# Kernel optimization log

Measured on AMD Instinct MI355X. Metric: run time of the kernel, lower is better.

The kernel has to match this reference:

```python
import jax, jax.numpy as jnp
import numpy as np

B, T, I, H, C = 32, 1024, 512, 1024, 512

def setup_inputs() -> dict:
    key = jax.random.key(0)
    ks = jax.random.split(key, 9)
    s_ih = 1.0 / np.sqrt(H)
    inp = {
        "x": jax.random.normal(ks[0], (B, T, I), dtype=jnp.float32),
        # LSTMCell params (PyTorch layout: [4H, in], gate order i,f,g,o)
        "W_ih": jax.random.uniform(ks[1], (4 * H, I), minval=-s_ih, maxval=s_ih, dtype=jnp.float32),
        "W_hh": jax.random.uniform(ks[2], (4 * H, H), minval=-s_ih, maxval=s_ih, dtype=jnp.float32),
        "b_ih": jax.random.uniform(ks[3], (4 * H,), minval=-s_ih, maxval=s_ih, dtype=jnp.float32),
        "b_hh": jax.random.uniform(ks[4], (4 * H,), minval=-s_ih, maxval=s_ih, dtype=jnp.float32),
        # fc head [C, H]
        "fc_w": jax.random.uniform(ks[5], (C, H), minval=-s_ih, maxval=s_ih, dtype=jnp.float32),
        "fc_b": jax.random.uniform(ks[6], (C,), minval=-s_ih, maxval=s_ih, dtype=jnp.float32),
        # ln_hidden [H, H] (reverse=False branch)
        "ln_w": jax.random.uniform(ks[7], (H, H), minval=-s_ih, maxval=s_ih, dtype=jnp.float32),
        "ln_b": jax.random.uniform(ks[8], (H,), minval=-s_ih, maxval=s_ih, dtype=jnp.float32),
    }
    return inp

def _lstm_forward(x, W_ih, W_hh, b_ih, b_hh):
    # Pre-compute input contribution for all timesteps: [B,T,4H]
    x_gates = jnp.einsum('bti,gi->btg', x, W_ih) + b_ih
    h0 = jnp.zeros((x.shape[0], H), dtype=x.dtype)
    c0 = jnp.zeros((x.shape[0], H), dtype=x.dtype)

    def step(carry, xg_t):
        h, c = carry
        gates = xg_t + h @ W_hh.T + b_hh  # [B,4H]
        i, f, g, o = jnp.split(gates, 4, axis=-1)
        c = jax.nn.sigmoid(f) * c + jax.nn.sigmoid(i) * jnp.tanh(g)
        h = jax.nn.sigmoid(o) * jnp.tanh(c)
        return (h, c), h

    (_, _), hs = jax.lax.scan(step, (h0, c0), jnp.swapaxes(x_gates, 0, 1))  # hs: [T,B,H]
    return jnp.swapaxes(hs, 0, 1)  # [B,T,H]

def reference(x, W_ih, W_hh, b_ih, b_hh, fc_w, fc_b, ln_w, ln_b):
    outputs = _lstm_forward(x, W_ih, W_hh, b_ih, b_hh)  # [B,T,H]
    out = jnp.einsum('bth,ch->btc', outputs, fc_w) + fc_b  # [B,T,C]
    # Faithful quirk: torch.stack(outputs, 1) on a [B,T,H] tensor -> [T,B,H]
    states_t = jnp.swapaxes(outputs, 0, 1)  # [T,B,H]
    states = jnp.einsum('tbh,gh->tbg', states_t, ln_w) + ln_b  # [T,B,H]
    return (out, states)
```

## Files before the change

kernel.cpp:

```cpp
#include <hip/hip_runtime.h>
#include <stdint.h>

#define B_  32
#define T_  1024
#define I_  512
#define H_  1024
#define C_  512
#define G4H 4096
#define NWG 128

typedef __bf16 bf16x8 __attribute__((ext_vector_type(8)));
typedef float  f32x4  __attribute__((ext_vector_type(4)));
typedef unsigned long long u64;

__device__ __forceinline__ unsigned short f2bf(float f) {
    uint32_t b = __float_as_uint(f);
    b = (b + 0x7FFFu + ((b >> 16) & 1u)) >> 16;
    return (unsigned short)b;
}
__device__ __forceinline__ float sigf(float x)   { return 1.0f / (1.0f + __expf(-x)); }
__device__ __forceinline__ float tanh_f(float x) { return 2.0f / (1.0f + __expf(-2.0f * x)) - 1.0f; }

__global__ void cvt_kernel(const float* __restrict__ src, unsigned short* __restrict__ dst, int n4) {
    int i = blockIdx.x * blockDim.x + threadIdx.x;
    if (i < n4) {
        float4 v = ((const float4*)src)[i];
        ushort4 o;
        o.x = f2bf(v.x); o.y = f2bf(v.y); o.z = f2bf(v.z); o.w = f2bf(v.w);
        ((ushort4*)dst)[i] = o;
    }
}

__global__ void cvt_x_kernel(const float* __restrict__ src, unsigned short* __restrict__ dst) {
    int i4 = blockIdx.x * blockDim.x + threadIdx.x;
    int b   = i4 / (T_ * I_ / 4);
    int rem = i4 % (T_ * I_ / 4);
    int t   = rem / (I_ / 4);
    int c4  = rem % (I_ / 4);
    float4 v = ((const float4*)src)[i4];
    ushort4 o;
    o.x = f2bf(v.x); o.y = f2bf(v.y); o.z = f2bf(v.z); o.w = f2bf(v.w);
    ((ushort4*)dst)[(t * B_ + b) * (I_ / 4) + c4] = o;
}

__global__ void bias_kernel(const float* __restrict__ a, const float* __restrict__ b, float* __restrict__ o) {
    int i = blockIdx.x * blockDim.x + threadIdx.x;
    if (i < G4H) o[i] = a[i] + b[i];
}

__global__ __launch_bounds__(512, 1) void lstm_rec(
        const unsigned short* __restrict__ whh,
        const unsigned short* __restrict__ wih,
        const unsigned short* __restrict__ xb,
        const float* __restrict__ bias,
        unsigned short* __restrict__ hall,
        unsigned int* __restrict__ flags)
{
    extern __shared__ char smem[];
    unsigned short* Wlds    = (unsigned short*)smem;
    float*          scratch = (float*)(smem + 98304);
    unsigned short* hstage  = (unsigned short*)(smem + 98304 + 32768);

    const int tid  = threadIdx.x;
    const int wg   = blockIdx.x;
    const int lane = tid & 63;
    const int wq   = tid >> 6;
    const int l15  = lane & 15;
    const int l4   = lane >> 4;

    for (int s = tid; s < 32 * 192; s += 512) {
        int col = s / 192, g = s % 192;
        int grow = (col >> 3) * H_ + wg * 8 + (col & 7);
        const unsigned short* src = (g < 128) ? (whh + grow * H_ + g * 8)
                                              : (wih + grow * I_ + (g - 128) * 8);
        int4 v = *(const int4*)src;
        int gd = g ^ (col & 7);
        *(int4*)(Wlds + col * 1536 + gd * 8) = v;
    }
    float bs0 = 0.f, bs1 = 0.f, bs2 = 0.f, bs3 = 0.f;
    if (tid < 256) {
        int u = tid & 7;
        bs0 = bias[0 * H_ + wg * 8 + u];
        bs1 = bias[1 * H_ + wg * 8 + u];
        bs2 = bias[2 * H_ + wg * 8 + u];
        bs3 = bias[3 * H_ + wg * 8 + u];
    }
    __syncthreads();

    float c_state = 0.0f;

    for (int t = 0; t < T_; ++t) {
        f32x4 acc[2][2];
        #pragma unroll
        for (int a = 0; a < 2; a++)
            #pragma unroll
            for (int b = 0; b < 2; b++) acc[a][b] = (f32x4){0.f, 0.f, 0.f, 0.f};

        #pragma unroll
        for (int kxs = 0; kxs < 2; kxs++) {
            int kk = wq * 64 + kxs * 32 + l4 * 8;
            bf16x8 af[2];
            #pragma unroll
            for (int mt = 0; mt < 2; mt++) {
                int bb = mt * 16 + l15;
                af[mt] = *(const bf16x8*)(xb + ((size_t)t * B_ + bb) * I_ + kk);
            }
            int gbase = 128 + (kk >> 3);
            bf16x8 bfr[2];
            #pragma unroll
            for (int nt = 0; nt < 2; nt++) {
                int col = nt * 16 + l15;
                int gg = gbase ^ (col & 7);
                bfr[nt] = *(const bf16x8*)(Wlds + col * 1536 + gg * 8);
            }
            #pragma unroll
            for (int mt = 0; mt < 2; mt++)
                #pragma unroll
                for (int nt = 0; nt < 2; nt++)
                    acc[mt][nt] = __builtin_amdgcn_mfma_f32_16x16x32_bf16(af[mt], bfr[nt], acc[mt][nt], 0, 0, 0);
        }

        if (t > 0) {
            if (tid < NWG) {
                const unsigned int* f = flags + ((size_t)(t - 1) * NWG + tid) * 16;
                while (__hip_atomic_load(f, __ATOMIC_RELAXED, __HIP_MEMORY_SCOPE_AGENT) == 0u)
                    __builtin_amdgcn_s_sleep(1);
            }
            __syncthreads();
            asm volatile("" ::: "memory");
        }

        const unsigned short* hprev = hall + (size_t)t * (B_ * H_);
        #pragma unroll
        for (int khs = 0; khs < 4; khs++) {
            int kk = wq * 128 + khs * 32 + l4 * 8;
            bf16x8 af[2];
            #pragma unroll
            for (int mt = 0; mt < 2; mt++) {
                int bb = mt * 16 + l15;
                af[mt] = *(const bf16x8*)(hprev + bb * H_ + kk);
            }
            int gbase = kk >> 3;
            bf16x8 bfr[2];
            #pragma unroll
            for (int nt = 0; nt < 2; nt++) {
                int col = nt * 16 + l15;
                int gg = gbase ^ (col & 7);
                bfr[nt] = *(const bf16x8*)(Wlds + col * 1536 + gg * 8);
            }
            #pragma unroll
            for (int mt = 0; mt < 2; mt++)
                #pragma unroll
                for (int nt = 0; nt < 2; nt++)
                    acc[mt][nt] = __builtin_amdgcn_mfma_f32_16x16x32_bf16(af[mt], bfr[nt], acc[mt][nt], 0, 0, 0);
        }

        float* myscr = scratch + wq * 1024;
        #pragma unroll
        for (int mt = 0; mt < 2; mt++)
            #pragma unroll
            for (int nt = 0; nt < 2; nt++)
                #pragma unroll
                for (int r = 0; r < 4; r++) {
                    int bb  = mt * 16 + l4 * 4 + r;
                    int col = nt * 16 + l15;
                    myscr[bb * 32 + (col ^ ((bb & 7) << 2))] = acc[mt][nt][r];
                }
        __syncthreads();

        if (tid < 256) {
            int bb = tid >> 3, u = tid & 7;
            int sw = (bb & 7) << 2;
            float p0 = bs0, p1 = bs1, p2 = bs2, p3 = bs3;
            const float* base = scratch + bb * 32;
            #pragma unroll
            for (int q = 0; q < 8; q++) {
                const float* sc = base + q * 1024;
                p0 += sc[(u)      ^ sw];
                p1 += sc[(8 + u)  ^ sw];
                p2 += sc[(16 + u) ^ sw];
                p3 += sc[(24 + u) ^ sw];
            }
            float ig = sigf(p0), fg = sigf(p1), gg = tanh_f(p2), og = sigf(p3);
            c_state = fg * c_state + ig * gg;
            float h = og * tanh_f(c_state);
            hstage[bb * 8 + u] = f2bf(h);
        }
        __syncthreads();

        if (tid < 64) {
            int bb = tid >> 1, part = tid & 1;
            u64 q = *(u64*)(hstage + bb * 8 + part * 4);
            u64* dst = (u64*)(hall + ((size_t)(t + 1) * B_ + bb) * H_ + wg * 8 + part * 4);
            __hip_atomic_store(dst, q, __ATOMIC_RELAXED, __HIP_MEMORY_SCOPE_AGENT);
        }
        __syncthreads();
        if (tid == 0)
            __hip_atomic_store(flags + ((size_t)t * NWG + wg) * 16, 1u,
                               __ATOMIC_RELAXED, __HIP_MEMORY_SCOPE_AGENT);
    }
}

template<int PERM>
__global__ __launch_bounds__(256) void gemm_bt(
        const unsigned short* __restrict__ A,
        const unsigned short* __restrict__ Bw,
        const float* __restrict__ bias,
        float* __restrict__ out)
{
    __shared__ unsigned short As[128 * 64];
    __shared__ unsigned short Bs[128 * 64];
    const int tid  = threadIdx.x;
    const int lane = tid & 63, w = tid >> 6;
    const int wm = w >> 1, wn = w & 1;
    const int mbase = blockIdx.y * 128, nbase = blockIdx.x * 128;
    const int l15 = lane & 15, l4 = lane >> 4;

    f32x4 acc[4][4];
    #pragma unroll
    for (int i = 0; i < 4; i++)
        #pragma unroll
        for (int j = 0; j < 4; j++) acc[i][j] = (f32x4){0.f, 0.f, 0.f, 0.f};

    for (int kb = 0; kb < 16; kb++) {
        __syncthreads();
        #pragma unroll
        for (int i = 0; i < 4; i++) {
            int s = i * 256 + tid;
            int row = s >> 3, g = s & 7;
            int gd = g ^ (row & 7);
            int4 va = *(const int4*)(A  + (size_t)(mbase + row) * 1024 + kb * 64 + g * 8);
            *(int4*)(As + row * 64 + gd * 8) = va;
            int4 vb = *(const int4*)(Bw + (size_t)(nbase + row) * 1024 + kb * 64 + g * 8);
            *(int4*)(Bs + row * 64 + gd * 8) = vb;
        }
        __syncthreads();
        #pragma unroll
        for (int kk = 0; kk < 2; kk++) {
            bf16x8 af[4], bf[4];
            #pragma unroll
            for (int mt = 0; mt < 4; mt++) {
                int row = wm * 64 + mt * 16 + l15;
                int gg = (kk * 4 + l4) ^ (row & 7);
                af[mt] = *(const bf16x8*)(As + row * 64 + gg * 8);
            }
            #pragma unroll
            for (int nt = 0; nt < 4; nt++) {
                int row = wn * 64 + nt * 16 + l15;
                int gg = (kk * 4 + l4) ^ (row & 7);
                bf[nt] = *(const bf16x8*)(Bs + row * 64 + gg * 8);
            }
            #pragma unroll
            for (int mt = 0; mt < 4; mt++)
                #pragma unroll
                for (int nt = 0; nt < 4; nt++)
                    acc[mt][nt] = __builtin_amdgcn_mfma_f32_16x16x32_bf16(af[mt], bf[nt], acc[mt][nt], 0, 0, 0);
        }
    }
    #pragma unroll
    for (int mt = 0; mt < 4; mt++)
        #pragma unroll
        for (int nt = 0; nt < 4; nt++)
            #pragma unroll
            for (int r = 0; r < 4; r++) {
                int grow = mbase + wm * 64 + mt * 16 + l4 * 4 + r;
                int gcol = nbase + wn * 64 + nt * 16 + l15;
                float v = acc[mt][nt][r] + bias[gcol];
                int idx;
                if (PERM == 1) {
                    int tt = grow >> 5, bb = grow & 31;
                    idx = (bb * 1024 + tt) * 512 + gcol;
                } else {
                    idx = grow * 1024 + gcol;
                }
                out[idx] = v;
            }
}

extern "C" void kernel_launch(void* const* d_in, const int* in_sizes, int n_in,
                              void* d_out, int out_size, void* d_ws, size_t ws_size,
                              hipStream_t stream) {
    (void)in_sizes; (void)n_in; (void)out_size; (void)ws_size;
    const float* x    = (const float*)d_in[0];
    const float* Wih  = (const float*)d_in[1];
    const float* Whh  = (const float*)d_in[2];
    const float* bih  = (const float*)d_in[3];
    const float* bhh  = (const float*)d_in[4];
    const float* fcw  = (const float*)d_in[5];
    const float* fcb  = (const float*)d_in[6];
    const float* lnw  = (const float*)d_in[7];
    const float* lnb  = (const float*)d_in[8];
    float* out = (float*)d_out;

    char* ws = (char*)d_ws;
    size_t o = 0;
    unsigned short* whh_b = (unsigned short*)(ws + o); o += 8388608;
    unsigned short* wih_b = (unsigned short*)(ws + o); o += 4194304;
    unsigned short* fcw_b = (unsigned short*)(ws + o); o += 1048576;
    unsigned short* lnw_b = (unsigned short*)(ws + o); o += 2097152;
    unsigned short* x_b   = (unsigned short*)(ws + o); o += 33554432;
    float*          bias_c = (float*)(ws + o);         o += 16384;
    unsigned short* hall  = (unsigned short*)(ws + o); o += 67174400;
    unsigned int*   flags = (unsigned int*)(ws + o);   o += 8388608;

    hipMemsetAsync(flags, 0, 8388608, stream);
    hipMemsetAsync(hall, 0, 65536, stream);

    cvt_kernel<<<4096,  256, 0, stream>>>(Whh, whh_b, 4194304 / 4);
    cvt_kernel<<<2048,  256, 0, stream>>>(Wih, wih_b, 2097152 / 4);
    cvt_kernel<<<512,   256, 0, stream>>>(fcw, fcw_b, 524288 / 4);
    cvt_kernel<<<1024,  256, 0, stream>>>(lnw, lnw_b, 1048576 / 4);
    cvt_x_kernel<<<16384, 256, 0, stream>>>(x, x_b);
    bias_kernel<<<16, 256, 0, stream>>>(bih, bhh, bias_c);

    const unsigned short* a0 = whh_b;
    const unsigned short* a1 = wih_b;
    const unsigned short* a2 = x_b;
    const float*          a3 = bias_c;
    unsigned short*       a4 = hall;
    unsigned int*         a5 = flags;
    void* args[6] = { (void*)&a0, (void*)&a1, (void*)&a2, (void*)&a3, (void*)&a4, (void*)&a5 };
    hipLaunchCooperativeKernel((void*)lstm_rec, dim3(NWG), dim3(512), args,
                               (unsigned)(98304 + 32768 + 512), stream);

    const unsigned short* hseq = hall + 32768;
    gemm_bt<1><<<dim3(4, 256), 256, 0, stream>>>(hseq, fcw_b, fcb, out);
    gemm_bt<2><<<dim3(8, 256), 256, 0, stream>>>(hseq, lnw_b, lnb, out + 16777216);
}
```

Before: 4.450 ms.

## Cut per-step barriers in LSTM recurrence with per-wave polling and counter

The W_ih slice now lives in registers rather than LDS, which shrinks the weight tile and frees LDS for a double-buffered scratch area indexed by timestep parity. Each wave now polls its own 16 producer flags instead of the block polling and then hitting a barrier. The two trailing barriers are replaced by per-wave stores of h, followed by an LDS atomic counter whose last arriver publishes the block's flag. This shortens the serial critical path of every timestep, at the cost of relying on subtle memory ordering (relaxed atomics, manual waitcnt) that may be fragile.

```diff
diff --git a/kernel.cpp b/kernel.cpp
--- a/kernel.cpp
+++ b/kernel.cpp
@@ -58,8 +58,9 @@
 {
     extern __shared__ char smem[];
     unsigned short* Wlds    = (unsigned short*)smem;
-    float*          scratch = (float*)(smem + 98304);
-    unsigned short* hstage  = (unsigned short*)(smem + 98304 + 32768);
+    float*          scratch = (float*)(smem + 65536);
+    unsigned short* hstage  = (unsigned short*)(smem + 131072);
+    int*            done    = (int*)(smem + 131584);
 
     const int tid  = threadIdx.x;
     const int wg   = blockIdx.x;
@@ -68,15 +69,22 @@
     const int l15  = lane & 15;
     const int l4   = lane >> 4;
 
-    for (int s = tid; s < 32 * 192; s += 512) {
-        int col = s / 192, g = s % 192;
+    for (int s = tid; s < 32 * 128; s += 512) {
+        int col = s >> 7, g = s & 127;
         int grow = (col >> 3) * H_ + wg * 8 + (col & 7);
-        const unsigned short* src = (g < 128) ? (whh + grow * H_ + g * 8)
-                                              : (wih + grow * I_ + (g - 128) * 8);
-        int4 v = *(const int4*)src;
-        int gd = g ^ (col & 7);
-        *(int4*)(Wlds + col * 1536 + gd * 8) = v;
-    }
+        int4 v = *(const int4*)(whh + (size_t)grow * H_ + g * 8);
+        *(int4*)(Wlds + col * 1024 + (g ^ (col & 7)) * 8) = v;
+    }
+    bf16x8 wfx[2][2];
+    #pragma unroll
+    for (int kxs = 0; kxs < 2; kxs++)
+        #pragma unroll
+        for (int nt = 0; nt < 2; nt++) {
+            int col = nt * 16 + l15;
+            int grow = (col >> 3) * H_ + wg * 8 + (col & 7);
+            int kk = wq * 64 + kxs * 32 + l4 * 8;
+            wfx[kxs][nt] = *(const bf16x8*)(wih + (size_t)grow * I_ + kk);
+        }
     float bs0 = 0.f, bs1 = 0.f, bs2 = 0.f, bs3 = 0.f;
     if (tid < 256) {
         int u = tid & 7;
@@ -85,6 +93,7 @@
         bs2 = bias[2 * H_ + wg * 8 + u];
         bs3 = bias[3 * H_ + wg * 8 + u];
     }
+    if (tid == 0) *done = 0;
     __syncthreads();
 
     float c_state = 0.0f;
@@ -105,13 +114,39 @@
                 int bb = mt * 16 + l15;
                 af[mt] = *(const bf16x8*)(xb + ((size_t)t * B_ + bb) * I_ + kk);
             }
-            int gbase = 128 + (kk >> 3);
+            #pragma unroll
+            for (int mt = 0; mt < 2; mt++)
+                #pragma unroll
+                for (int nt = 0; nt < 2; nt++)
+                    acc[mt][nt] = __builtin_amdgcn_mfma_f32_16x16x32_bf16(af[mt], wfx[kxs][nt], acc[mt][nt], 0, 0, 0);
+        }
+
+        if (t > 0) {
+            if (lane < 16) {
+                const unsigned int* f = flags + ((size_t)(t - 1) * NWG + wq * 16 + lane) * 16;
+                while (__hip_atomic_load(f, __ATOMIC_RELAXED, __HIP_MEMORY_SCOPE_AGENT) == 0u)
+                    __builtin_amdgcn_s_sleep(1);
+            }
+            asm volatile("" ::: "memory");
+        }
+
+        const unsigned short* hprev = hall + (size_t)t * (B_ * H_);
+        #pragma unroll
+        for (int khs = 0; khs < 4; khs++) {
+            int kk = wq * 128 + khs * 32 + l4 * 8;
+            bf16x8 af[2];
+            #pragma unroll
+            for (int mt = 0; mt < 2; mt++) {
+                int bb = mt * 16 + l15;
+                af[mt] = *(const bf16x8*)(hprev + bb * H_ + kk);
+            }
+            int gbase = kk >> 3;
             bf16x8 bfr[2];
             #pragma unroll
             for (int nt = 0; nt < 2; nt++) {
                 int col = nt * 16 + l15;
                 int gg = gbase ^ (col & 7);
-                bfr[nt] = *(const bf16x8*)(Wlds + col * 1536 + gg * 8);
+                bfr[nt] = *(const bf16x8*)(Wlds + col * 1024 + gg * 8);
             }
             #pragma unroll
             for (int mt = 0; mt < 2; mt++)
@@ -120,42 +155,7 @@
                     acc[mt][nt] = __builtin_amdgcn_mfma_f32_16x16x32_bf16(af[mt], bfr[nt], acc[mt][nt], 0, 0, 0);
         }
 
-        if (t > 0) {
-            if (tid < NWG) {
-                const unsigned int* f = flags + ((size_t)(t - 1) * NWG + tid) * 16;
-                while (__hip_atomic_load(f, __ATOMIC_RELAXED, __HIP_MEMORY_SCOPE_AGENT) == 0u)
-                    __builtin_amdgcn_s_sleep(1);
-            }
-            __syncthreads();
-            asm volatile("" ::: "memory");
-        }
-
-        const unsigned short* hprev = hall + (size_t)t * (B_ * H_);
-        #pragma unroll
-        for (int khs = 0; khs < 4; khs++) {
-            int kk = wq * 128 + khs * 32 + l4 * 8;
-            bf16x8 af[2];
-            #pragma unroll
-            for (int mt = 0; mt < 2; mt++) {
-                int bb = mt * 16 + l15;
-                af[mt] = *(const bf16x8*)(hprev + bb * H_ + kk);
-            }
-            int gbase = kk >> 3;
-            bf16x8 bfr[2];
-            #pragma unroll
-            for (int nt = 0; nt < 2; nt++) {
-                int col = nt * 16 + l15;
-                int gg = gbase ^ (col & 7);
-                bfr[nt] = *(const bf16x8*)(Wlds + col * 1536 + gg * 8);
-            }
-            #pragma unroll
-            for (int mt = 0; mt < 2; mt++)
-                #pragma unroll
-                for (int nt = 0; nt < 2; nt++)
-                    acc[mt][nt] = __builtin_amdgcn_mfma_f32_16x16x32_bf16(af[mt], bfr[nt], acc[mt][nt], 0, 0, 0);
-        }
-
-        float* myscr = scratch + wq * 1024;
+        float* myscr = scratch + (t & 1) * 8192 + wq * 1024;
         #pragma unroll
         for (int mt = 0; mt < 2; mt++)
             #pragma unroll
@@ -172,7 +172,7 @@
             int bb = tid >> 3, u = tid & 7;
             int sw = (bb & 7) << 2;
             float p0 = bs0, p1 = bs1, p2 = bs2, p3 = bs3;
-            const float* base = scratch + bb * 32;
+            const float* base = scratch + (t & 1) * 8192 + bb * 32;
             #pragma unroll
             for (int q = 0; q < 8; q++) {
                 const float* sc = base + q * 1024;
@@ -185,19 +185,22 @@
             c_state = fg * c_state + ig * gg;
             float h = og * tanh_f(c_state);
             hstage[bb * 8 + u] = f2bf(h);
-        }
-        __syncthreads();
-
-        if (tid < 64) {
-            int bb = tid >> 1, part = tid & 1;
-            u64 q = *(u64*)(hstage + bb * 8 + part * 4);
-            u64* dst = (u64*)(hall + ((size_t)(t + 1) * B_ + bb) * H_ + wg * 8 + part * 4);
-            __hip_atomic_store(dst, q, __ATOMIC_RELAXED, __HIP_MEMORY_SCOPE_AGENT);
-        }
-        __syncthreads();
-        if (tid == 0)
-            __hip_atomic_store(flags + ((size_t)t * NWG + wg) * 16, 1u,
-                               __ATOMIC_RELAXED, __HIP_MEMORY_SCOPE_AGENT);
+            asm volatile("s_waitcnt lgkmcnt(0)" ::: "memory");
+
+            if (lane < 16) {
+                int pb = wq * 8 + (lane >> 1), part = lane & 1;
+                u64 q = *(const u64*)(hstage + pb * 8 + part * 4);
+                u64* dst = (u64*)(hall + ((size_t)(t + 1) * B_ + pb) * H_ + wg * 8 + part * 4);
+                __hip_atomic_store(dst, q, __ATOMIC_RELAXED, __HIP_MEMORY_SCOPE_AGENT);
+            }
+            asm volatile("s_waitcnt vmcnt(0)" ::: "memory");
+            if (lane == 0) {
+                int old = __hip_atomic_fetch_add(done, 1, __ATOMIC_RELAXED, __HIP_MEMORY_SCOPE_WORKGROUP);
+                if (old == t * 4 + 3)
+                    __hip_atomic_store(flags + ((size_t)t * NWG + wg) * 16, 1u,
+                                       __ATOMIC_RELAXED, __HIP_MEMORY_SCOPE_AGENT);
+            }
+        }
     }
 }
 
@@ -321,7 +324,7 @@
     unsigned int*         a5 = flags;
     void* args[6] = { (void*)&a0, (void*)&a1, (void*)&a2, (void*)&a3, (void*)&a4, (void*)&a5 };
     hipLaunchCooperativeKernel((void*)lstm_rec, dim3(NWG), dim3(512), args,
-                               (unsigned)(98304 + 32768 + 512), stream);
+                               (unsigned)131600, stream);
 
     const unsigned short* hseq = hall + 32768;
     gemm_bt<1><<<dim3(4, 256), 256, 0, stream>>>(hseq, fcw_b, fcb, out);
```

New measurement: 4.403 ms. No clear change (-1.0%).
